# Optimization experiments

Measured on AMD Instinct MI355X. Metric: run time of the kernel, lower is better.

## Reference

```python
import jax, jax.numpy as jnp
import numpy as np

HEADS = 2
NEG_SLOPE = 0.2  # PyG GATConv default leaky_relu slope


def gat_conv(x, edge_index, W, a_src, a_dst, bias, num_nodes):
    """PyG-style GATConv with concat=True and self-loops.
    x: [N, Fin], W: [Fin, H*C], a_src/a_dst: [H, C], bias: [H*C].
    edge_index: [2, E] with row 0 = source j, row 1 = target i.
    """
    H = HEADS
    C = W.shape[1] // H
    # add self loops
    loops = jnp.arange(num_nodes, dtype=edge_index.dtype)
    src = jnp.concatenate([edge_index[0], loops])
    dst = jnp.concatenate([edge_index[1], loops])

    xW = (x @ W).reshape(num_nodes, H, C)            # [N, H, C]
    alpha_s = jnp.einsum('nhc,hc->nh', xW, a_src)    # [N, H]
    alpha_d = jnp.einsum('nhc,hc->nh', xW, a_dst)    # [N, H]
    e = alpha_s[src] + alpha_d[dst]                  # [E, H]
    e = jax.nn.leaky_relu(e, NEG_SLOPE)
    # segment softmax over edges sharing the same target node
    m = jax.ops.segment_max(e, dst, num_segments=num_nodes)  # [N, H]
    e = jnp.exp(e - m[dst])
    denom = jax.ops.segment_sum(e, dst, num_segments=num_nodes)  # [N, H]
    alpha = e / denom[dst]                           # [E, H]
    # message = alpha_ij * xW_j, aggregated at target i
    msg = xW[src] * alpha[:, :, None]                # [E, H, C]
    out = jax.ops.segment_sum(msg, dst, num_segments=num_nodes)  # [N, H, C]
    return out.reshape(num_nodes, H * C) + bias


def setup_inputs() -> dict:
    key = jax.random.key(0)
    ks = jax.random.split(key, 10)
    N, E = 50000, 800000
    Fin, D = 128, 128
    H = HEADS
    x = jax.random.normal(ks[0], (N, Fin), dtype=jnp.float32)
    edge_index = jax.random.randint(ks[1], (2, E), 0, N, dtype=jnp.int64)
    g = 1.0 / np.sqrt(Fin)
    W1 = jax.random.normal(ks[2], (Fin, H * D), dtype=jnp.float32) * g
    a_src1 = jax.random.normal(ks[3], (H, D), dtype=jnp.float32) * g
    a_dst1 = jax.random.normal(ks[4], (H, D), dtype=jnp.float32) * g
    b1 = jnp.zeros((H * D,), dtype=jnp.float32)
    g2 = 1.0 / np.sqrt(H * D)
    W2 = jax.random.normal(ks[5], (H * D, H * D), dtype=jnp.float32) * g2
    a_src2 = jax.random.normal(ks[6], (H, D), dtype=jnp.float32) * g2
    a_dst2 = jax.random.normal(ks[7], (H, D), dtype=jnp.float32) * g2
    b2 = jnp.zeros((H * D,), dtype=jnp.float32)
    return {"x": x, "edge_index": edge_index,
            "W1": W1, "a_src1": a_src1, "a_dst1": a_dst1, "b1": b1,
            "W2": W2, "a_src2": a_src2, "a_dst2": a_dst2, "b2": b2}


def reference(x, edge_index, W1, a_src1, a_dst1, b1, W2, a_src2, a_dst2, b2):
    N = x.shape[0]
    h = gat_conv(x, edge_index, W1, a_src1, a_dst1, b1, N)
    h = jax.nn.elu(h)
    # dropout is identity in eval mode (deterministic reference)
    out = gat_conv(h, edge_index, W2, a_src2, a_dst2, b2, N)
    return out
```

## Files before the change

### kernel.cpp

```cpp
#include <hip/hip_runtime.h>
#include <math.h>

#define HEADS 2
#define CH    128
#define HC    256
#define NEG   0.2f

typedef __attribute__((ext_vector_type(8))) short  bfrag8;
typedef __attribute__((ext_vector_type(4))) float  f32x4;

__device__ inline unsigned short f2bf_rne(float x) {
    unsigned u = __float_as_uint(x);
    u += 0x7fffu + ((u >> 16) & 1u);
    return (unsigned short)(u >> 16);
}
__device__ inline void split2(float x, unsigned short& hi, unsigned short& lo) {
    unsigned u = __float_as_uint(x);
    unsigned r = u + 0x7fffu + ((u >> 16) & 1u);
    unsigned short h = (unsigned short)(r >> 16);
    float hf = __uint_as_float((unsigned)h << 16);
    hi = h;
    lo = f2bf_rne(x - hf);
}

__global__ __launch_bounds__(256)
void wsplit_kernel(const float* __restrict__ W, unsigned short* __restrict__ Whi,
                   unsigned short* __restrict__ Wlo, int K) {
    const int idx = blockIdx.x * 256 + threadIdx.x;
    if (idx >= K * HC) return;
    const int k = idx >> 8;
    const int n = idx & 255;
    unsigned short h, l;
    split2(W[idx], h, l);
    Whi[(size_t)n * K + k] = h;
    Wlo[(size_t)n * K + k] = l;
}

__global__ __launch_bounds__(256)
void gemm_mfma_kernel(const float* __restrict__ A,
                      const unsigned short* __restrict__ Wthi,
                      const unsigned short* __restrict__ Wtlo,
                      float* __restrict__ C, int M, int K) {
    __shared__ unsigned short Ah[128][40];
    __shared__ unsigned short Al[128][40];
    __shared__ unsigned short Bh[128][40];
    __shared__ unsigned short Bl[128][40];

    const int t    = threadIdx.x;
    const int row0 = blockIdx.x * 128;
    const int col0 = blockIdx.y * 128;
    const int lane = t & 63;
    const int wid  = t >> 6;
    const int wr   = wid >> 1;
    const int wc   = wid & 1;

    f32x4 acc[4][4] = {};

    const int ar  = t >> 3;
    const int ac4 = (t & 7) * 4;
    const int bcol   = t >> 1;
    const int bplane = t & 1;

    for (int kk = 0; kk < K; kk += 32) {
        #pragma unroll
        for (int rep = 0; rep < 4; ++rep) {
            const int row = ar + rep * 32;
            const int gr  = row0 + row;
            float4 v = make_float4(0.f, 0.f, 0.f, 0.f);
            if (gr < M)
                v = *reinterpret_cast<const float4*>(&A[(size_t)gr * K + kk + ac4]);
            ushort4 hv, lv;
            split2(v.x, hv.x, lv.x);
            split2(v.y, hv.y, lv.y);
            split2(v.z, hv.z, lv.z);
            split2(v.w, hv.w, lv.w);
            *reinterpret_cast<ushort4*>(&Ah[row][ac4]) = hv;
            *reinterpret_cast<ushort4*>(&Al[row][ac4]) = lv;
        }
        {
            const unsigned short* srcp =
                (bplane ? Wtlo : Wthi) + (size_t)(col0 + bcol) * K + kk;
            unsigned short (*dst)[40] = bplane ? Bl : Bh;
            #pragma unroll
            for (int q = 0; q < 4; ++q) {
                bfrag8 v = *reinterpret_cast<const bfrag8*>(srcp + q * 8);
                *reinterpret_cast<bfrag8*>(&dst[bcol][q * 8]) = v;
            }
        }
        __syncthreads();

        bfrag8 ah[4], al[4], bh[4], bl[4];
        const int ko = (lane >> 4) * 8;
        #pragma unroll
        for (int m = 0; m < 4; ++m) {
            const int row = wr * 64 + m * 16 + (lane & 15);
            ah[m] = *reinterpret_cast<const bfrag8*>(&Ah[row][ko]);
            al[m] = *reinterpret_cast<const bfrag8*>(&Al[row][ko]);
        }
        #pragma unroll
        for (int n = 0; n < 4; ++n) {
            const int col = wc * 64 + n * 16 + (lane & 15);
            bh[n] = *reinterpret_cast<const bfrag8*>(&Bh[col][ko]);
            bl[n] = *reinterpret_cast<const bfrag8*>(&Bl[col][ko]);
        }

        #pragma unroll
        for (int m = 0; m < 4; ++m)
            #pragma unroll
            for (int n = 0; n < 4; ++n) {
                acc[m][n] = __builtin_amdgcn_mfma_f32_16x16x32_bf16(al[m], bh[n], acc[m][n], 0, 0, 0);
                acc[m][n] = __builtin_amdgcn_mfma_f32_16x16x32_bf16(ah[m], bl[n], acc[m][n], 0, 0, 0);
                acc[m][n] = __builtin_amdgcn_mfma_f32_16x16x32_bf16(ah[m], bh[n], acc[m][n], 0, 0, 0);
            }
        __syncthreads();
    }

    #pragma unroll
    for (int m = 0; m < 4; ++m) {
        #pragma unroll
        for (int reg = 0; reg < 4; ++reg) {
            const int gr = row0 + wr * 64 + m * 16 + (lane >> 4) * 4 + reg;
            if (gr < M) {
                #pragma unroll
                for (int n = 0; n < 4; ++n) {
                    const int gc = col0 + wc * 64 + n * 16 + (lane & 15);
                    C[(size_t)gr * HC + gc] = acc[m][n][reg];
                }
            }
        }
    }
}

__global__ __launch_bounds__(256)
void alpha_kernel(const float* __restrict__ xW, const float* __restrict__ a_src,
                  const float* __restrict__ a_dst, float* __restrict__ as_out,
                  float* __restrict__ ad_out, unsigned short* __restrict__ xWb,
                  int N) {
    const int wid  = (blockIdx.x * 256 + threadIdx.x) >> 6;
    const int lane = threadIdx.x & 63;
    if (wid >= N) return;
    const int h  = lane >> 5;
    const int c0 = (lane & 31) * 4;
    const float4 v  = *reinterpret_cast<const float4*>(&xW[(size_t)wid * HC + lane * 4]);
    ushort4 bv;
    bv.x = f2bf_rne(v.x); bv.y = f2bf_rne(v.y);
    bv.z = f2bf_rne(v.z); bv.w = f2bf_rne(v.w);
    *reinterpret_cast<ushort4*>(&xWb[(size_t)wid * HC + lane * 4]) = bv;

    const float4 s4 = *reinterpret_cast<const float4*>(&a_src[h * CH + c0]);
    const float4 d4 = *reinterpret_cast<const float4*>(&a_dst[h * CH + c0]);
    float s = v.x * s4.x + v.y * s4.y + v.z * s4.z + v.w * s4.w;
    float d = v.x * d4.x + v.y * d4.y + v.z * d4.z + v.w * d4.w;
    #pragma unroll
    for (int m = 1; m <= 16; m <<= 1) {
        s += __shfl_xor(s, m);
        d += __shfl_xor(d, m);
    }
    if ((lane & 31) == 0) {
        as_out[wid * 2 + h] = s;
        ad_out[wid * 2 + h] = d;
    }
}

__global__ __launch_bounds__(256)
void hist_kernel(const int* __restrict__ dst, int* __restrict__ counts, int E) {
    const int e = blockIdx.x * 256 + threadIdx.x;
    if (e < E) atomicAdd(&counts[dst[e]], 1);
}

__global__ __launch_bounds__(256)
void scan_local_kernel(int* __restrict__ data, int* __restrict__ chunk_sum, int N) {
    __shared__ int s[256];
    const int t   = threadIdx.x;
    const int idx = blockIdx.x * 256 + t;
    const int v   = (idx < N) ? data[idx] : 0;
    s[t] = v;
    __syncthreads();
    #pragma unroll
    for (int off = 1; off < 256; off <<= 1) {
        int x = (t >= off) ? s[t - off] : 0;
        __syncthreads();
        s[t] += x;
        __syncthreads();
    }
    if (idx < N) data[idx] = s[t] - v;
    if (t == 255) chunk_sum[blockIdx.x] = s[255];
}

__global__ __launch_bounds__(256)
void scan_chunks_kernel(int* __restrict__ chunk, int nb) {
    __shared__ int s[256];
    const int t = threadIdx.x;
    const int v = (t < nb) ? chunk[t] : 0;
    s[t] = v;
    __syncthreads();
    #pragma unroll
    for (int off = 1; off < 256; off <<= 1) {
        int x = (t >= off) ? s[t - off] : 0;
        __syncthreads();
        s[t] += x;
        __syncthreads();
    }
    if (t < nb) chunk[t] = s[t] - v;
}

__global__ __launch_bounds__(256)
void add_offsets_kernel(const int* __restrict__ excl, const int* __restrict__ chunk_excl,
                        int* __restrict__ row_ptr, int* __restrict__ cursor,
                        int N, int E) {
    const int idx = blockIdx.x * 256 + threadIdx.x;
    if (idx < N) {
        const int rp = excl[idx] + chunk_excl[idx >> 8];
        row_ptr[idx] = rp;
        cursor[idx]  = rp;
    }
    if (idx == 0) row_ptr[N] = E;
}

__global__ __launch_bounds__(256)
void scatter_kernel(const int* __restrict__ src, const int* __restrict__ dst,
                    int* __restrict__ cursor, int* __restrict__ col_idx, int E) {
    const int e = blockIdx.x * 256 + threadIdx.x;
    if (e < E) {
        const int pos = atomicAdd(&cursor[dst[e]], 1);
        col_idx[pos] = src[e];
    }
}

__global__ __launch_bounds__(256)
void agg_kernel(const int* __restrict__ row_ptr, const int* __restrict__ col_idx,
                const float* __restrict__ xW, const unsigned short* __restrict__ xWb,
                const float* __restrict__ as_, const float* __restrict__ ad_,
                const float* __restrict__ bias, float* __restrict__ out,
                int N, int do_elu) {
    const int wv   = (blockIdx.x * 256 + threadIdx.x) >> 6;
    const int lane = threadIdx.x & 63;
    if (wv >= N) return;
    const int i    = wv;
    const int half = lane >> 5;
    const int sl   = lane & 31;
    const int hh   = sl >> 4;
    const int cb   = hh * 128 + (sl & 15) * 8;
    const float adi = ad_[i * 2 + hh];

    float acc[8] = {};
    float dn = 0.f;

    const int beg = row_ptr[i];
    const int end = row_ptr[i + 1];

    int k = beg + half;
    int j = (k < end) ? col_idx[k] : 0;
    for (; k < end; k += 2) {
        const int jn = (k + 2 < end) ? col_idx[k + 2] : 0;
        float e = as_[j * 2 + hh] + adi;
        e = e > 0.f ? e : NEG * e;
        const float w = expf(e);
        const uint4 q = *reinterpret_cast<const uint4*>(&xWb[(size_t)j * HC + cb]);
        const unsigned qq[4] = {q.x, q.y, q.z, q.w};
        #pragma unroll
        for (int r = 0; r < 4; ++r) {
            const float flo = __uint_as_float(qq[r] << 16);
            const float fhi = __uint_as_float(qq[r] & 0xffff0000u);
            acc[r * 2 + 0] = fmaf(w, flo, acc[r * 2 + 0]);
            acc[r * 2 + 1] = fmaf(w, fhi, acc[r * 2 + 1]);
        }
        dn += w;
        j = jn;
    }

    #pragma unroll
    for (int r = 0; r < 8; ++r) acc[r] += __shfl_xor(acc[r], 32);
    dn += __shfl_xor(dn, 32);

    if (lane < 32) {
        float e = as_[i * 2 + hh] + adi;
        e = e > 0.f ? e : NEG * e;
        const float ws = expf(e);
        const float4 v0 = *reinterpret_cast<const float4*>(&xW[(size_t)i * HC + cb]);
        const float4 v1 = *reinterpret_cast<const float4*>(&xW[(size_t)i * HC + cb + 4]);
        acc[0] = fmaf(ws, v0.x, acc[0]); acc[1] = fmaf(ws, v0.y, acc[1]);
        acc[2] = fmaf(ws, v0.z, acc[2]); acc[3] = fmaf(ws, v0.w, acc[3]);
        acc[4] = fmaf(ws, v1.x, acc[4]); acc[5] = fmaf(ws, v1.y, acc[5]);
        acc[6] = fmaf(ws, v1.z, acc[6]); acc[7] = fmaf(ws, v1.w, acc[7]);
        dn += ws;

        const float inv = 1.f / dn;
        const float4 b0 = *reinterpret_cast<const float4*>(&bias[cb]);
        const float4 b1 = *reinterpret_cast<const float4*>(&bias[cb + 4]);
        float o[8];
        o[0] = acc[0] * inv + b0.x; o[1] = acc[1] * inv + b0.y;
        o[2] = acc[2] * inv + b0.z; o[3] = acc[3] * inv + b0.w;
        o[4] = acc[4] * inv + b1.x; o[5] = acc[5] * inv + b1.y;
        o[6] = acc[6] * inv + b1.z; o[7] = acc[7] * inv + b1.w;
        if (do_elu) {
            #pragma unroll
            for (int r = 0; r < 8; ++r) o[r] = o[r] > 0.f ? o[r] : expm1f(o[r]);
        }
        *reinterpret_cast<float4*>(&out[(size_t)i * HC + cb]) =
            make_float4(o[0], o[1], o[2], o[3]);
        *reinterpret_cast<float4*>(&out[(size_t)i * HC + cb + 4]) =
            make_float4(o[4], o[5], o[6], o[7]);
    }
}

extern "C" void kernel_launch(void* const* d_in, const int* in_sizes, int n_in,
                              void* d_out, int out_size, void* d_ws, size_t ws_size,
                              hipStream_t stream) {
    const float* x      = (const float*)d_in[0];
    const int*   ei     = (const int*)d_in[1];
    const float* W1     = (const float*)d_in[2];
    const float* a_src1 = (const float*)d_in[3];
    const float* a_dst1 = (const float*)d_in[4];
    const float* b1     = (const float*)d_in[5];
    const float* W2     = (const float*)d_in[6];
    const float* a_src2 = (const float*)d_in[7];
    const float* a_dst2 = (const float*)d_in[8];
    const float* b2     = (const float*)d_in[9];
    float* out = (float*)d_out;

    const int Nn = in_sizes[0] / 128;
    const int E  = in_sizes[1] / 2;
    const int K1 = in_sizes[2] / HC;
    const int* src = ei;
    const int* dst = ei + E;

    float* bufA  = (float*)d_ws;
    float* bufB  = bufA + (size_t)Nn * HC;
    float* as_b  = bufB + (size_t)Nn * HC;
    float* ad_b  = as_b + (size_t)Nn * 2;
    int*   tmp   = (int*)(ad_b + (size_t)Nn * 2);
    int*   chunk = tmp + Nn;
    int*   rowp  = chunk + 256;
    int*   curs  = rowp + (Nn + 1);
    int*   colx  = curs + Nn;
    unsigned short* wt1hi = (unsigned short*)(colx + E);
    unsigned short* wt1lo = wt1hi + (size_t)HC * K1;
    unsigned short* wt2hi = wt1lo + (size_t)HC * K1;
    unsigned short* wt2lo = wt2hi + (size_t)HC * HC;
    unsigned short* xWb   = wt2lo + (size_t)HC * HC;

    const int nb = (Nn + 255) / 256;

    wsplit_kernel<<<(K1 * HC + 255) / 256, 256, 0, stream>>>(W1, wt1hi, wt1lo, K1);
    wsplit_kernel<<<(HC * HC + 255) / 256, 256, 0, stream>>>(W2, wt2hi, wt2lo, HC);

    hipMemsetAsync(tmp, 0, (size_t)Nn * sizeof(int), stream);
    hist_kernel<<<(E + 255) / 256, 256, 0, stream>>>(dst, tmp, E);
    scan_local_kernel<<<nb, 256, 0, stream>>>(tmp, chunk, Nn);
    scan_chunks_kernel<<<1, 256, 0, stream>>>(chunk, nb);
    add_offsets_kernel<<<nb, 256, 0, stream>>>(tmp, chunk, rowp, curs, Nn, E);
    scatter_kernel<<<(E + 255) / 256, 256, 0, stream>>>(src, dst, curs, colx, E);

    const dim3 ggrid((Nn + 127) / 128, HC / 128);
    const int  agrid = (Nn + 3) / 4;

    gemm_mfma_kernel<<<ggrid, 256, 0, stream>>>(x, wt1hi, wt1lo, bufA, Nn, K1);
    alpha_kernel<<<agrid, 256, 0, stream>>>(bufA, a_src1, a_dst1, as_b, ad_b, xWb, Nn);
    agg_kernel<<<agrid, 256, 0, stream>>>(rowp, colx, bufA, xWb, as_b, ad_b, b1, bufB, Nn, 1);

    gemm_mfma_kernel<<<ggrid, 256, 0, stream>>>(bufB, wt2hi, wt2lo, bufA, Nn, HC);
    alpha_kernel<<<agrid, 256, 0, stream>>>(bufA, a_src2, a_dst2, as_b, ad_b, xWb, Nn);
    agg_kernel<<<agrid, 256, 0, stream>>>(rowp, colx, bufA, xWb, as_b, ad_b, b2, out, Nn, 0);
}
```

Measured before the change: 382.5 us.

## Fuse attention-coefficient and bf16 conversion into GEMM epilogue

The GEMM epilogue now computes per-row source/destination attention logits via in-wave shuffles and LDS reduction, and writes only a bf16 copy of xW, eliminating the separate alpha kernel and the fp32 xW buffer. The aggregation kernel's self-loop term reads the bf16 copy instead of fp32. This removes a full fp32 write and read of the projected features per layer, at the cost of slightly lower precision for the self-loop contribution and a heavier epilogue.

```diff
diff --git a/kernel.cpp b/kernel.cpp
--- a/kernel.cpp
+++ b/kernel.cpp
@@ -37,10 +37,14 @@
 }
 
 __global__ __launch_bounds__(256)
-void gemm_mfma_kernel(const float* __restrict__ A,
-                      const unsigned short* __restrict__ Wthi,
-                      const unsigned short* __restrict__ Wtlo,
-                      float* __restrict__ C, int M, int K) {
+void gemm_fused_kernel(const float* __restrict__ A,
+                       const unsigned short* __restrict__ Wthi,
+                       const unsigned short* __restrict__ Wtlo,
+                       const float* __restrict__ a_src,
+                       const float* __restrict__ a_dst,
+                       unsigned short* __restrict__ xWb,
+                       float* __restrict__ as_out, float* __restrict__ ad_out,
+                       int M, int K) {
     __shared__ unsigned short Ah[128][40];
     __shared__ unsigned short Al[128][40];
     __shared__ unsigned short Bh[128][40];
@@ -115,50 +119,51 @@
         __syncthreads();
     }
 
+    __shared__ float s_lds[2][128];
+    __shared__ float d_lds[2][128];
+
+    float asv[4], adv[4];
+    #pragma unroll
+    for (int n = 0; n < 4; ++n) {
+        const int gc = col0 + wc * 64 + n * 16 + (lane & 15);
+        asv[n] = a_src[gc];
+        adv[n] = a_dst[gc];
+    }
+
     #pragma unroll
     for (int m = 0; m < 4; ++m) {
         #pragma unroll
         for (int reg = 0; reg < 4; ++reg) {
-            const int gr = row0 + wr * 64 + m * 16 + (lane >> 4) * 4 + reg;
+            const int row = wr * 64 + m * 16 + (lane >> 4) * 4 + reg;
+            const int gr  = row0 + row;
+            float ps = acc[m][0][reg] * asv[0] + acc[m][1][reg] * asv[1] +
+                       acc[m][2][reg] * asv[2] + acc[m][3][reg] * asv[3];
+            float pd = acc[m][0][reg] * adv[0] + acc[m][1][reg] * adv[1] +
+                       acc[m][2][reg] * adv[2] + acc[m][3][reg] * adv[3];
+            #pragma unroll
+            for (int msk = 1; msk <= 8; msk <<= 1) {
+                ps += __shfl_xor(ps, msk);
+                pd += __shfl_xor(pd, msk);
+            }
+            if ((lane & 15) == 0) {
+                s_lds[wc][row] = ps;
+                d_lds[wc][row] = pd;
+            }
             if (gr < M) {
+                unsigned short* rp = &xWb[(size_t)gr * HC + col0];
                 #pragma unroll
-                for (int n = 0; n < 4; ++n) {
-                    const int gc = col0 + wc * 64 + n * 16 + (lane & 15);
-                    C[(size_t)gr * HC + gc] = acc[m][n][reg];
-                }
-            }
-        }
-    }
-}
-
-__global__ __launch_bounds__(256)
-void alpha_kernel(const float* __restrict__ xW, const float* __restrict__ a_src,
-                  const float* __restrict__ a_dst, float* __restrict__ as_out,
-                  float* __restrict__ ad_out, unsigned short* __restrict__ xWb,
-                  int N) {
-    const int wid  = (blockIdx.x * 256 + threadIdx.x) >> 6;
-    const int lane = threadIdx.x & 63;
-    if (wid >= N) return;
-    const int h  = lane >> 5;
-    const int c0 = (lane & 31) * 4;
-    const float4 v  = *reinterpret_cast<const float4*>(&xW[(size_t)wid * HC + lane * 4]);
-    ushort4 bv;
-    bv.x = f2bf_rne(v.x); bv.y = f2bf_rne(v.y);
-    bv.z = f2bf_rne(v.z); bv.w = f2bf_rne(v.w);
-    *reinterpret_cast<ushort4*>(&xWb[(size_t)wid * HC + lane * 4]) = bv;
-
-    const float4 s4 = *reinterpret_cast<const float4*>(&a_src[h * CH + c0]);
-    const float4 d4 = *reinterpret_cast<const float4*>(&a_dst[h * CH + c0]);
-    float s = v.x * s4.x + v.y * s4.y + v.z * s4.z + v.w * s4.w;
-    float d = v.x * d4.x + v.y * d4.y + v.z * d4.z + v.w * d4.w;
-    #pragma unroll
-    for (int m = 1; m <= 16; m <<= 1) {
-        s += __shfl_xor(s, m);
-        d += __shfl_xor(d, m);
-    }
-    if ((lane & 31) == 0) {
-        as_out[wid * 2 + h] = s;
-        ad_out[wid * 2 + h] = d;
+                for (int n = 0; n < 4; ++n)
+                    rp[wc * 64 + n * 16 + (lane & 15)] = f2bf_rne(acc[m][n][reg]);
+            }
+        }
+    }
+    __syncthreads();
+    if (t < 128) {
+        const int gr = row0 + t;
+        if (gr < M) {
+            as_out[gr * 2 + blockIdx.y] = s_lds[0][t] + s_lds[1][t];
+            ad_out[gr * 2 + blockIdx.y] = d_lds[0][t] + d_lds[1][t];
+        }
     }
 }
 
@@ -229,7 +234,7 @@
 
 __global__ __launch_bounds__(256)
 void agg_kernel(const int* __restrict__ row_ptr, const int* __restrict__ col_idx,
-                const float* __restrict__ xW, const unsigned short* __restrict__ xWb,
+                const unsigned short* __restrict__ xWb,
                 const float* __restrict__ as_, const float* __restrict__ ad_,
                 const float* __restrict__ bias, float* __restrict__ out,
                 int N, int do_elu) {
@@ -277,12 +282,15 @@
         float e = as_[i * 2 + hh] + adi;
         e = e > 0.f ? e : NEG * e;
         const float ws = expf(e);
-        const float4 v0 = *reinterpret_cast<const float4*>(&xW[(size_t)i * HC + cb]);
-        const float4 v1 = *reinterpret_cast<const float4*>(&xW[(size_t)i * HC + cb + 4]);
-        acc[0] = fmaf(ws, v0.x, acc[0]); acc[1] = fmaf(ws, v0.y, acc[1]);
-        acc[2] = fmaf(ws, v0.z, acc[2]); acc[3] = fmaf(ws, v0.w, acc[3]);
-        acc[4] = fmaf(ws, v1.x, acc[4]); acc[5] = fmaf(ws, v1.y, acc[5]);
-        acc[6] = fmaf(ws, v1.z, acc[6]); acc[7] = fmaf(ws, v1.w, acc[7]);
+        const uint4 q = *reinterpret_cast<const uint4*>(&xWb[(size_t)i * HC + cb]);
+        const unsigned qq[4] = {q.x, q.y, q.z, q.w};
+        #pragma unroll
+        for (int r = 0; r < 4; ++r) {
+            const float flo = __uint_as_float(qq[r] << 16);
+            const float fhi = __uint_as_float(qq[r] & 0xffff0000u);
+            acc[r * 2 + 0] = fmaf(ws, flo, acc[r * 2 + 0]);
+            acc[r * 2 + 1] = fmaf(ws, fhi, acc[r * 2 + 1]);
+        }
         dn += ws;
 
         const float inv = 1.f / dn;
@@ -325,8 +333,7 @@
     const int* src = ei;
     const int* dst = ei + E;
 
-    float* bufA  = (float*)d_ws;
-    float* bufB  = bufA + (size_t)Nn * HC;
+    float* bufB  = (float*)d_ws;
     float* as_b  = bufB + (size_t)Nn * HC;
     float* ad_b  = as_b + (size_t)Nn * 2;
     int*   tmp   = (int*)(ad_b + (size_t)Nn * 2);
@@ -355,11 +362,11 @@
     const dim3 ggrid((Nn + 127) / 128, HC / 128);
     const int  agrid = (Nn + 3) / 4;
 
-    gemm_mfma_kernel<<<ggrid, 256, 0, stream>>>(x, wt1hi, wt1lo, bufA, Nn, K1);
-    alpha_kernel<<<agrid, 256, 0, stream>>>(bufA, a_src1, a_dst1, as_b, ad_b, xWb, Nn);
-    agg_kernel<<<agrid, 256, 0, stream>>>(rowp, colx, bufA, xWb, as_b, ad_b, b1, bufB, Nn, 1);
-
-    gemm_mfma_kernel<<<ggrid, 256, 0, stream>>>(bufB, wt2hi, wt2lo, bufA, Nn, HC);
-    alpha_kernel<<<agrid, 256, 0, stream>>>(bufA, a_src2, a_dst2, as_b, ad_b, xWb, Nn);
-    agg_kernel<<<agrid, 256, 0, stream>>>(rowp, colx, bufA, xWb, as_b, ad_b, b2, out, Nn, 0);
-}
+    gemm_fused_kernel<<<ggrid, 256, 0, stream>>>(x, wt1hi, wt1lo, a_src1, a_dst1,
+                                                 xWb, as_b, ad_b, Nn, K1);
+    agg_kernel<<<agrid, 256, 0, stream>>>(rowp, colx, xWb, as_b, ad_b, b1, bufB, Nn, 1);
+
+    gemm_fused_kernel<<<ggrid, 256, 0, stream>>>(bufB, wt2hi, wt2lo, a_src2, a_dst2,
+                                                 xWb, as_b, ad_b, Nn, HC);
+    agg_kernel<<<agrid, 256, 0, stream>>>(rowp, colx, xWb, as_b, ad_b, b2, out, Nn, 0);
+}
```

Result: faster. 352.2 us (-7.9%).
